# Kernel optimization log

Measured on AMD Instinct MI355X. Metric: run time of the kernel, lower is better.

The kernel has to match this reference:

```python
import jax, jax.numpy as jnp
import numpy as np

EPS = 1e-5  # BatchNorm2d default eps


def _conv3x3(x, w):
    # x: [B,C,H,W], w: [O,I,3,3], stride 1, 'same' padding (autopad k=3 -> p=1)
    return jax.lax.conv_general_dilated(
        x, w, window_strides=(1, 1), padding=((1, 1), (1, 1)),
        dimension_numbers=("NCHW", "OIHW", "NCHW"))


def _bn(x, g, b, m, v):
    # inference-mode BatchNorm2d with materialized running stats
    scale = (g / jnp.sqrt(v + EPS))[None, :, None, None]
    return (x - m[None, :, None, None]) * scale + b[None, :, None, None]


def _silu(x):
    return x * jax.nn.sigmoid(x)


def _pam(y, q_w, q_b, k_w, k_b, v_w, v_b, pam_gamma):
    # PAM_Module: full pixel-wise self-attention over N = H*W tokens
    B, C, H, W = y.shape
    N = H * W
    yf = y.reshape(B, C, N)
    # 1x1 convs expressed as channel matmuls; q_w: [C//8, C], v_w: [C, C]
    q = jnp.einsum("oc,bcn->bno", q_w, yf) + q_b                 # [B, N, C//8]
    k = jnp.einsum("oc,bcn->bon", k_w, yf) + k_b[None, :, None]  # [B, C//8, N]
    v = jnp.einsum("oc,bcn->bon", v_w, yf) + v_b[None, :, None]  # [B, C, N]
    energy = jnp.einsum("bno,bom->bnm", q, k)                    # [B, N, N]
    attn = jax.nn.softmax(energy, axis=-1)
    # torch: bmm(v, attn.permute(0,2,1)) -> out[b,c,n] = sum_m v[b,c,m] * attn[b,n,m]
    out = jnp.einsum("bcm,bnm->bcn", v, attn).reshape(B, C, H, W)
    return pam_gamma * out + y


def setup_inputs() -> dict:
    key = jax.random.key(0)
    ks = jax.random.split(key, 16)
    B, C1, C2, H, W = 4, 64, 64, 64, 64
    C_ = C2 // 2          # e = 0.5
    C8 = C2 // 8          # PAM q/k channels
    s = 0.05
    inp = {
        "x": jax.random.normal(ks[0], (B, C1, H, W), jnp.float32),
        # cv1: Conv(c1, c_, 3, 1)
        "cv1_w": jax.random.normal(ks[1], (C_, C1, 3, 3), jnp.float32) * s,
        "bn1_g": jax.random.uniform(ks[2], (C_,), jnp.float32, 0.5, 1.5),
        "bn1_b": jax.random.normal(ks[3], (C_,), jnp.float32) * s,
        "bn1_m": jax.random.normal(ks[4], (C_,), jnp.float32) * s,
        "bn1_v": jax.random.uniform(ks[5], (C_,), jnp.float32, 0.5, 1.5),
        # cv2: Conv(c_, c2, 3, 1)
        "cv2_w": jax.random.normal(ks[6], (C2, C_, 3, 3), jnp.float32) * s,
        "bn2_g": jax.random.uniform(ks[7], (C2,), jnp.float32, 0.5, 1.5),
        "bn2_b": jax.random.normal(ks[8], (C2,), jnp.float32) * s,
        "bn2_m": jax.random.normal(ks[9], (C2,), jnp.float32) * s,
        "bn2_v": jax.random.uniform(ks[10], (C2,), jnp.float32, 0.5, 1.5),
        # PAM 1x1 convs (flattened kernels) + biases + gamma
        "q_w": jax.random.normal(ks[11], (C8, C2), jnp.float32) * s,
        "q_b": jax.random.normal(ks[12], (C8,), jnp.float32) * s,
        "k_w": jax.random.normal(ks[13], (C8, C2), jnp.float32) * s,
        "k_b": jax.random.normal(ks[14], (C8,), jnp.float32) * s,
        "v_w": jax.random.normal(ks[15], (C2, C2), jnp.float32) * s,
        "v_b": jnp.zeros((C2,), jnp.float32),
        "pam_gamma": jnp.float32(0.5),  # torch inits 0 (identity); nonzero to exercise path
    }
    return inp


def reference(x, cv1_w, bn1_g, bn1_b, bn1_m, bn1_v,
              cv2_w, bn2_g, bn2_b, bn2_m, bn2_v,
              q_w, q_b, k_w, k_b, v_w, v_b, pam_gamma):
    y = _silu(_bn(_conv3x3(x, cv1_w), bn1_g, bn1_b, bn1_m, bn1_v))   # cv1
    y = _silu(_bn(_conv3x3(y, cv2_w), bn2_g, bn2_b, bn2_m, bn2_v))   # cv2
    # SAA: PAM applied twice on identical input and summed == 2 * PAM(y)
    att = 2.0 * _pam(y, q_w, q_b, k_w, k_b, v_w, v_b, pam_gamma)
    return x + att  # shortcut active (c1 == c2)
```

## Files before the change

### kernel.cpp

```cpp
#include <hip/hip_runtime.h>
#include <hip/hip_bf16.h>

#define NB 4
#define NN 4096

typedef short  bf16x8 __attribute__((ext_vector_type(8)));
typedef float  f32x4  __attribute__((ext_vector_type(4)));

static __device__ __forceinline__ ushort f2bf(float f) {
    unsigned u = __float_as_uint(f);
    u += 0x7fffu + ((u >> 16) & 1u);
    return (ushort)(u >> 16);
}
static __device__ __forceinline__ float bflo(unsigned w) { return __uint_as_float(w << 16); }
static __device__ __forceinline__ float bfhi(unsigned w) { return __uint_as_float(w & 0xffff0000u); }

__global__ __launch_bounds__(256) void prep(
    const float* __restrict__ x, const float* __restrict__ w1, const float* __restrict__ w2,
    ushort* __restrict__ xt, ushort* __restrict__ W1r, ushort* __restrict__ W2r)
{
    const int tid = threadIdx.x;
    const int blk = blockIdx.x;
    if (blk < 256) {
        __shared__ float Ts[64][66];
        const int b = blk >> 6, n0 = (blk & 63) * 64;
        const int wv = tid >> 6, lane = tid & 63;
        #pragma unroll
        for (int i = 0; i < 16; ++i) {
            int ci = i * 4 + wv, nn = lane;
            Ts[ci][nn] = x[((size_t)b * 64 + ci) * NN + n0 + nn];
        }
        __syncthreads();
        #pragma unroll
        for (int i = 0; i < 16; ++i) {
            int nn = i * 4 + wv, ci = lane;
            xt[((size_t)b * NN + n0 + nn) * 64 + ci] = f2bf(Ts[ci][nn]);
        }
    } else if (blk < 258) {
        const int base = (blk - 256) * 9216;
        #pragma unroll
        for (int i = 0; i < 36; ++i) {
            int e = base + i * 256 + tid;
            int co = e / 576, k = e % 576, tap = k >> 6, ci = k & 63;
            W1r[e] = f2bf(w1[((size_t)co * 64 + ci) * 9 + tap]);
        }
    } else {
        const int base = (blk - 258) * 9216;
        #pragma unroll
        for (int i = 0; i < 36; ++i) {
            int e = base + i * 256 + tid;
            int co = e / 288, k = e % 288, tap = k >> 5, ci = k & 31;
            W2r[e] = f2bf(w2[((size_t)co * 32 + ci) * 9 + tap]);
        }
    }
}

__global__ __launch_bounds__(256) void conv1_mfma(
    const ushort* __restrict__ xt, const ushort* __restrict__ W1r,
    const float* __restrict__ bng, const float* __restrict__ bnb,
    const float* __restrict__ bnm, const float* __restrict__ bnv,
    ushort* __restrict__ y1t)
{
    __shared__ __align__(16) ushort As[32 * 600];
    __shared__ __align__(16) ushort Xs[24 * 66 * 8];

    const int tid = threadIdx.x;
    const int h = blockIdx.x, b = blockIdx.y;

    #pragma unroll
    for (int i = 0; i < 9; ++i) {
        int cid = i * 256 + tid;
        int row = cid / 72, off = cid % 72;
        *(uint4*)&As[row * 600 + off * 8] = *(const uint4*)(W1r + (size_t)cid * 8);
    }
    #pragma unroll
    for (int r = 0; r < 3; ++r) {
        int gh = h - 1 + r;
        #pragma unroll
        for (int i = 0; i < 2; ++i) {
            int cid = i * 256 + tid;
            int w_ = cid >> 3, cc = cid & 7;
            uint4 v = {0, 0, 0, 0};
            if ((unsigned)gh < 64u)
                v = *(const uint4*)(xt + ((size_t)(b * NN + gh * 64) * 64) + (size_t)cid * 8);
            *(uint4*)&Xs[((r * 8 + cc) * 66 + (w_ + 1)) * 8] = v;
        }
    }
    if (tid < 48) {
        int r = tid >> 4, q = tid & 15, cc = q >> 1, side = (q & 1) * 65;
        uint4 z = {0, 0, 0, 0};
        *(uint4*)&Xs[((r * 8 + cc) * 66 + side) * 8] = z;
    }
    __syncthreads();

    const int lane = tid & 63, wv = tid >> 6;
    const int quad = lane >> 4, l15 = lane & 15;
    const int ch = wv & 1, ph = wv >> 1;

    f32x4 acc[2] = {{0.f,0.f,0.f,0.f},{0.f,0.f,0.f,0.f}};
    #pragma unroll
    for (int kk = 0; kk < 18; ++kk) {
        const int tap = kk >> 1;
        const int dyr = tap / 3, dx = tap % 3;
        bf16x8 af = *(const bf16x8*)&As[(ch * 16 + l15) * 600 + kk * 32 + quad * 8];
        #pragma unroll
        for (int s = 0; s < 2; ++s) {
            int p = ph * 32 + s * 16 + l15;
            bf16x8 bf = *(const bf16x8*)&Xs[((dyr * 8 + (kk & 1) * 4 + quad) * 66 + p + dx) * 8];
            acc[s] = __builtin_amdgcn_mfma_f32_16x16x32_bf16(af, bf, acc[s], 0, 0, 0);
        }
    }

    const int cb = ch * 16 + quad * 4;
    float sc[4], bs[4];
    #pragma unroll
    for (int r = 0; r < 4; ++r) {
        int co = cb + r;
        sc[r] = bng[co] / sqrtf(bnv[co] + 1e-5f);
        bs[r] = bnb[co] - bnm[co] * sc[r];
    }
    #pragma unroll
    for (int s = 0; s < 2; ++s) {
        int p = ph * 32 + s * 16 + l15;
        ushort u4[4];
        #pragma unroll
        for (int r = 0; r < 4; ++r) {
            float pre = acc[s][r] * sc[r] + bs[r];
            u4[r] = f2bf(pre / (1.f + __expf(-pre)));
        }
        *(uint2*)&y1t[((size_t)(b * NN + h * 64 + p)) * 32 + cb] = *(uint2*)u4;
    }
}

__global__ __launch_bounds__(256) void conv2qkv(
    const ushort* __restrict__ y1t, const ushort* __restrict__ W2r,
    const float* __restrict__ bng, const float* __restrict__ bnb,
    const float* __restrict__ bnm, const float* __restrict__ bnv,
    const float* __restrict__ qw, const float* __restrict__ qb,
    const float* __restrict__ kw, const float* __restrict__ kb,
    const float* __restrict__ vw, const float* __restrict__ vb,
    float* __restrict__ y, ushort* __restrict__ q8,
    ushort* __restrict__ ko, ushort* __restrict__ vt)
{
    __shared__ __align__(16) ushort As[64 * 312];
    __shared__ __align__(16) ushort Xs[12 * 66 * 8];
    __shared__ __align__(16) ushort Yt[64 * 76];
    __shared__ __align__(16) ushort Wq[80 * 76];
    __shared__ float Bv[80];

    const int tid = threadIdx.x;
    const int h = blockIdx.x, b = blockIdx.y;

    #pragma unroll
    for (int i = 0; i < 9; ++i) {
        int cid = i * 256 + tid;
        int row = cid / 36, off = cid % 36;
        *(uint4*)&As[row * 312 + off * 8] = *(const uint4*)(W2r + (size_t)cid * 8);
    }
    #pragma unroll
    for (int r = 0; r < 3; ++r) {
        int gh = h - 1 + r;
        int cid = tid;
        int w_ = cid >> 2, cc = cid & 3;
        uint4 v = {0, 0, 0, 0};
        if ((unsigned)gh < 64u)
            v = *(const uint4*)(y1t + ((size_t)(b * NN + gh * 64) * 32) + (size_t)cid * 8);
        *(uint4*)&Xs[((r * 4 + cc) * 66 + (w_ + 1)) * 8] = v;
    }
    if (tid < 24) {
        int r = tid >> 3, q = tid & 7, cc = q >> 1, side = (q & 1) * 65;
        uint4 z = {0, 0, 0, 0};
        *(uint4*)&Xs[((r * 4 + cc) * 66 + side) * 8] = z;
    }
    for (int i = tid; i < 2560; i += 256) {
        int chw = i >> 5, c2 = (i & 31) * 2;
        const float* src = (chw < 8) ? (qw + chw * 64 + c2)
                         : (chw < 16) ? (kw + (chw - 8) * 64 + c2)
                         : (vw + (chw - 16) * 64 + c2);
        float2 v2 = *(const float2*)src;
        *(unsigned*)&Wq[chw * 76 + c2] = ((unsigned)f2bf(v2.y) << 16) | f2bf(v2.x);
    }
    if (tid < 80) Bv[tid] = (tid < 8) ? qb[tid] : (tid < 16) ? kb[tid - 8] : vb[tid - 16];
    __syncthreads();

    const int lane = tid & 63, wv = tid >> 6;
    const int quad = lane >> 4, l15 = lane & 15;

    f32x4 acc[4] = {{0.f,0.f,0.f,0.f},{0.f,0.f,0.f,0.f},{0.f,0.f,0.f,0.f},{0.f,0.f,0.f,0.f}};
    #pragma unroll
    for (int kk = 0; kk < 9; ++kk) {
        const int dyr = kk / 3, dx = kk % 3;
        bf16x8 af = *(const bf16x8*)&As[(wv * 16 + l15) * 312 + kk * 32 + quad * 8];
        #pragma unroll
        for (int s = 0; s < 4; ++s) {
            int p = s * 16 + l15;
            bf16x8 bf = *(const bf16x8*)&Xs[((dyr * 4 + quad) * 66 + p + dx) * 8];
            acc[s] = __builtin_amdgcn_mfma_f32_16x16x32_bf16(af, bf, acc[s], 0, 0, 0);
        }
    }

    const int cb = wv * 16 + quad * 4;
    float sc[4], bs[4];
    #pragma unroll
    for (int r = 0; r < 4; ++r) {
        int co = cb + r;
        sc[r] = bng[co] / sqrtf(bnv[co] + 1e-5f);
        bs[r] = bnb[co] - bnm[co] * sc[r];
    }
    #pragma unroll
    for (int s = 0; s < 4; ++s) {
        int p = s * 16 + l15;
        #pragma unroll
        for (int r = 0; r < 4; ++r) {
            float pre = acc[s][r] * sc[r] + bs[r];
            float res = pre / (1.f + __expf(-pre));
            y[((size_t)(b * 64 + cb + r)) * NN + h * 64 + p] = res;
            Yt[p * 76 + cb + r] = f2bf(res);
        }
    }
    __syncthreads();

    bf16x8 aY0 = *(const bf16x8*)&Yt[(wv * 16 + l15) * 76 + quad * 8];
    bf16x8 aY1 = *(const bf16x8*)&Yt[(wv * 16 + l15) * 76 + 32 + quad * 8];
    const int nbase = h * 64 + wv * 16 + quad * 4;
    const int vslot = h * 64 + (wv >> 1) * 32 + quad * 8 + (wv & 1) * 4;
    #pragma unroll
    for (int cht = 0; cht < 5; ++cht) {
        bf16x8 bW0 = *(const bf16x8*)&Wq[(cht * 16 + l15) * 76 + quad * 8];
        bf16x8 bW1 = *(const bf16x8*)&Wq[(cht * 16 + l15) * 76 + 32 + quad * 8];
        f32x4 qa = {0.f, 0.f, 0.f, 0.f};
        qa = __builtin_amdgcn_mfma_f32_16x16x32_bf16(aY0, bW0, qa, 0, 0, 0);
        qa = __builtin_amdgcn_mfma_f32_16x16x32_bf16(aY1, bW1, qa, 0, 0, 0);
        const float bias = Bv[cht * 16 + l15];
        const int chn = cht * 16 + l15;
        if (cht == 0) {
            if (l15 < 8) {
                #pragma unroll
                for (int r = 0; r < 4; ++r)
                    q8[((size_t)b * NN + nbase + r) * 8 + chn] = f2bf(qa[r] + bias);
            } else {
                #pragma unroll
                for (int r = 0; r < 4; ++r)
                    ko[((size_t)b * NN + nbase + r) * 8 + (chn - 8)] = f2bf(qa[r] + bias);
            }
        } else {
            const int c = chn - 16;
            ushort u4[4];
            #pragma unroll
            for (int r = 0; r < 4; ++r) u4[r] = f2bf(qa[r] + bias);
            *(uint2*)&vt[((size_t)b * 64 + c) * NN + vslot] = *(uint2*)u4;
        }
    }
}

__global__ __launch_bounds__(256, 4) void flash_pam_split(
    const ushort* __restrict__ q8,
    const ushort* __restrict__ k8,
    const ushort* __restrict__ vt,
    ushort* __restrict__ O0, ushort* __restrict__ O1,
    float* __restrict__ lpart)
{
    __shared__ __align__(16) float Osum[4 * 2304];
    __shared__ float Lw[4][32];

    const int tid = threadIdx.x;
    const int bx = blockIdx.x;
    const int b  = bx >> 8;
    const int nt = (bx >> 1) & 127;
    const int sp = bx & 1;
    const int n0 = nt * 32;
    const int mb = sp * 2048;

    const int lane = tid & 63, w = tid >> 6;
    const int quad = lane >> 4, l15 = lane & 15;

    const uint4 z4 = {0u, 0u, 0u, 0u};

    bf16x8 bQ[2];
    #pragma unroll
    for (int af = 0; af < 2; ++af) {
        uint4 qv = *(const uint4*)(q8 + ((size_t)b * NN + n0 + af * 16 + l15) * 8);
        uint4 sel = (quad == 0) ? qv : z4;
        bQ[af] = *(bf16x8*)&sel;
    }

    const ushort* kg = k8 + ((size_t)b * NN + mb + w * 512) * 8;
    const ushort* vg = vt + (size_t)b * 64 * NN + mb + w * 512;

    f32x4 acc[2][4] = {{{0.f,0.f,0.f,0.f},{0.f,0.f,0.f,0.f},{0.f,0.f,0.f,0.f},{0.f,0.f,0.f,0.f}},
                       {{0.f,0.f,0.f,0.f},{0.f,0.f,0.f,0.f},{0.f,0.f,0.f,0.f},{0.f,0.f,0.f,0.f}}};
    float lacc[2] = {0.f, 0.f};
    const f32x4 zf = {0.f, 0.f, 0.f, 0.f};

    #pragma unroll 2
    for (int t = 0; t < 16; ++t) {
        const int g = t * 32;
        uint4 k0r = *(const uint4*)(kg + (size_t)(g + l15) * 8);
        uint4 k1r = *(const uint4*)(kg + (size_t)(g + 16 + l15) * 8);
        uint4 k0s = (quad == 0) ? k0r : z4;
        uint4 k1s = (quad == 0) ? k1r : z4;
        bf16x8 aK0 = *(bf16x8*)&k0s;
        bf16x8 aK1 = *(bf16x8*)&k1s;

        bf16x8 vb_[4];
        #pragma unroll
        for (int ct = 0; ct < 4; ++ct)
            vb_[ct] = *(const bf16x8*)(vg + (size_t)(ct * 16 + l15) * NN + g + quad * 8);

        f32x4 s0[2], s1[2];
        #pragma unroll
        for (int af = 0; af < 2; ++af) {
            s0[af] = __builtin_amdgcn_mfma_f32_16x16x32_bf16(aK0, bQ[af], zf, 0, 0, 0);
            s1[af] = __builtin_amdgcn_mfma_f32_16x16x32_bf16(aK1, bQ[af], zf, 0, 0, 0);
        }

        bf16x8 pa[2];
        #pragma unroll
        for (int af = 0; af < 2; ++af) {
            union { ushort u[8]; bf16x8 v; } pk;
            #pragma unroll
            for (int r = 0; r < 4; ++r) {
                float e = __expf(s0[af][r]);
                lacc[af] += e;
                pk.u[r] = f2bf(e);
            }
            #pragma unroll
            for (int r = 0; r < 4; ++r) {
                float e = __expf(s1[af][r]);
                lacc[af] += e;
                pk.u[4 + r] = f2bf(e);
            }
            pa[af] = pk.v;
        }

        #pragma unroll
        for (int af = 0; af < 2; ++af)
            #pragma unroll
            for (int ct = 0; ct < 4; ++ct)
                acc[af][ct] = __builtin_amdgcn_mfma_f32_16x16x32_bf16(pa[af], vb_[ct], acc[af][ct], 0, 0, 0);
    }

    #pragma unroll
    for (int af = 0; af < 2; ++af) {
        lacc[af] += __shfl_xor(lacc[af], 16, 64);
        lacc[af] += __shfl_xor(lacc[af], 32, 64);
    }
    if (quad == 0) {
        Lw[w][l15]      = lacc[0];
        Lw[w][16 + l15] = lacc[1];
    }

    #pragma unroll
    for (int af = 0; af < 2; ++af)
        #pragma unroll
        for (int ct = 0; ct < 4; ++ct)
            *(f32x4*)&Osum[w * 2304 + (ct * 16 + l15) * 36 + af * 16 + quad * 4] = acc[af][ct];
    __syncthreads();

    if (tid < 32)
        lpart[((size_t)(sp * 4 + b)) * NN + n0 + tid] =
            Lw[0][tid] + Lw[1][tid] + Lw[2][tid] + Lw[3][tid];

    ushort* Od = sp ? O1 : O0;
    const int nn = tid & 31, cq = tid >> 5;
    #pragma unroll
    for (int u = 0; u < 8; ++u) {
        int c = cq * 8 + u;
        float v = Osum[0 * 2304 + c * 36 + nn] + Osum[1 * 2304 + c * 36 + nn]
                + Osum[2 * 2304 + c * 36 + nn] + Osum[3 * 2304 + c * 36 + nn];
        Od[((size_t)b * 64 + c) * NN + n0 + nn] = f2bf(v);
    }
}

__global__ __launch_bounds__(256) void merge_out(
    const ushort* __restrict__ O0, const ushort* __restrict__ O1,
    const float* __restrict__ lpart,
    const float* __restrict__ x, const float* __restrict__ y,
    const float* __restrict__ gamma_p, float* __restrict__ out)
{
    const size_t base4 = ((size_t)blockIdx.x * 256 + threadIdx.x) * 4;
    const int n = (int)(base4 & 4095);
    const int b = (int)(base4 >> 18);
    const float g2 = 2.f * gamma_p[0];

    uint2 r0 = *(const uint2*)(O0 + base4);
    uint2 r1 = *(const uint2*)(O1 + base4);
    const float* l0 = lpart + (size_t)b * NN + n;
    const float* l1 = lpart + (size_t)(4 + b) * NN + n;

    f32x4 o;
    o[0] = bflo(r0.x) + bflo(r1.x);
    o[1] = bfhi(r0.x) + bfhi(r1.x);
    o[2] = bflo(r0.y) + bflo(r1.y);
    o[3] = bfhi(r0.y) + bfhi(r1.y);

    f32x4 xv = *(const f32x4*)(x + base4);
    f32x4 yv = *(const f32x4*)(y + base4);
    f32x4 res;
    #pragma unroll
    for (int u = 0; u < 4; ++u)
        res[u] = xv[u] + 2.f * yv[u] + g2 * o[u] / (l0[u] + l1[u]);
    *(f32x4*)(out + base4) = res;
}

extern "C" void kernel_launch(void* const* d_in, const int* in_sizes, int n_in,
                              void* d_out, int out_size, void* d_ws, size_t ws_size,
                              hipStream_t stream) {
    const float* x    = (const float*)d_in[0];
    const float* w1   = (const float*)d_in[1];
    const float* g1   = (const float*)d_in[2];
    const float* b1   = (const float*)d_in[3];
    const float* m1   = (const float*)d_in[4];
    const float* v1   = (const float*)d_in[5];
    const float* w2   = (const float*)d_in[6];
    const float* g2   = (const float*)d_in[7];
    const float* b2   = (const float*)d_in[8];
    const float* m2   = (const float*)d_in[9];
    const float* v2   = (const float*)d_in[10];
    const float* qw   = (const float*)d_in[11];
    const float* qb   = (const float*)d_in[12];
    const float* kw   = (const float*)d_in[13];
    const float* kb   = (const float*)d_in[14];
    const float* vw   = (const float*)d_in[15];
    const float* vb   = (const float*)d_in[16];
    const float* gam  = (const float*)d_in[17];
    float* outp = (float*)d_out;

    float* ws = (float*)d_ws;
    ushort* xt  = (ushort*)ws;
    float*  y   = ws + 524288;
    ushort* q8  = (ushort*)(ws + 1572864);
    ushort* kk  = (ushort*)(ws + 1703936);
    ushort* vv  = (ushort*)(ws + 1769472);
    float*  lp  = ws + 2293760;
    float*  S   = ws + 2326528;
    ushort* y1t = (ushort*)S;
    ushort* W1r = (ushort*)(S + 262144);
    ushort* W2r = (ushort*)(S + 271360);
    ushort* O0  = (ushort*)S;
    ushort* O1  = xt;

    prep<<<260, 256, 0, stream>>>(x, w1, w2, xt, W1r, W2r);
    conv1_mfma<<<dim3(64, NB), 256, 0, stream>>>(xt, W1r, g1, b1, m1, v1, y1t);
    conv2qkv<<<dim3(64, NB), 256, 0, stream>>>(y1t, W2r, g2, b2, m2, v2,
                                               qw, qb, kw, kb, vw, vb,
                                               y, q8, kk, vv);
    flash_pam_split<<<1024, 256, 0, stream>>>(q8, kk, vv, O0, O1, lp);
    merge_out<<<1024, 256, 0, stream>>>(O0, O1, lp, x, y, gam, outp);
}
```

Before: 149.8 us.

## Fuse split-KV merge and residual epilogue into single 8-wave flash PAM kernel

Replaces the two-way key split plus separate merge kernel with one kernel of 512 threads, where 8 waves each cover 512 keys and reduce their partial outputs and row sums in shared memory. The epilogue applies the normalization, gamma scaling and residual adds directly, removing the bf16 partial-output round trip through global memory and one kernel launch. In exchange the grid halves to 512 blocks of 512 threads and shared memory per block doubles to about 74 KB, which lowers occupancy and may leave compute units underused.

Measured after the change: 143.4 us. 4.3% less time.

```diff
diff --git a/kernel.cpp b/kernel.cpp
--- a/kernel.cpp
+++ b/kernel.cpp
@@ -12,8 +12,6 @@
     u += 0x7fffu + ((u >> 16) & 1u);
     return (ushort)(u >> 16);
 }
-static __device__ __forceinline__ float bflo(unsigned w) { return __uint_as_float(w << 16); }
-static __device__ __forceinline__ float bfhi(unsigned w) { return __uint_as_float(w & 0xffff0000u); }
 
 __global__ __launch_bounds__(256) void prep(
     const float* __restrict__ x, const float* __restrict__ w1, const float* __restrict__ w2,
@@ -253,23 +251,24 @@
     }
 }
 
-__global__ __launch_bounds__(256, 4) void flash_pam_split(
+__global__ __launch_bounds__(512, 4) void flash_pam(
     const ushort* __restrict__ q8,
     const ushort* __restrict__ k8,
     const ushort* __restrict__ vt,
-    ushort* __restrict__ O0, ushort* __restrict__ O1,
-    float* __restrict__ lpart)
+    const float* __restrict__ y,
+    const float* __restrict__ x,
+    const float* __restrict__ gamma_p,
+    float* __restrict__ out)
 {
-    __shared__ __align__(16) float Osum[4 * 2304];
-    __shared__ float Lw[4][32];
+    __shared__ __align__(16) float Osum[8 * 2304];
+    __shared__ float Lw[8][32];
+    __shared__ float Ls[32];
 
     const int tid = threadIdx.x;
     const int bx = blockIdx.x;
-    const int b  = bx >> 8;
-    const int nt = (bx >> 1) & 127;
-    const int sp = bx & 1;
+    const int b  = bx >> 7;
+    const int nt = bx & 127;
     const int n0 = nt * 32;
-    const int mb = sp * 2048;
 
     const int lane = tid & 63, w = tid >> 6;
     const int quad = lane >> 4, l15 = lane & 15;
@@ -284,8 +283,8 @@
         bQ[af] = *(bf16x8*)&sel;
     }
 
-    const ushort* kg = k8 + ((size_t)b * NN + mb + w * 512) * 8;
-    const ushort* vg = vt + (size_t)b * 64 * NN + mb + w * 512;
+    const ushort* kg = k8 + ((size_t)b * NN + w * 512) * 8;
+    const ushort* vg = vt + (size_t)b * 64 * NN + w * 512;
 
     f32x4 acc[2][4] = {{{0.f,0.f,0.f,0.f},{0.f,0.f,0.f,0.f},{0.f,0.f,0.f,0.f},{0.f,0.f,0.f,0.f}},
                        {{0.f,0.f,0.f,0.f},{0.f,0.f,0.f,0.f},{0.f,0.f,0.f,0.f},{0.f,0.f,0.f,0.f}}};
@@ -357,50 +356,26 @@
             *(f32x4*)&Osum[w * 2304 + (ct * 16 + l15) * 36 + af * 16 + quad * 4] = acc[af][ct];
     __syncthreads();
 
-    if (tid < 32)
-        lpart[((size_t)(sp * 4 + b)) * NN + n0 + tid] =
-            Lw[0][tid] + Lw[1][tid] + Lw[2][tid] + Lw[3][tid];
-
-    ushort* Od = sp ? O1 : O0;
-    const int nn = tid & 31, cq = tid >> 5;
-    #pragma unroll
-    for (int u = 0; u < 8; ++u) {
-        int c = cq * 8 + u;
-        float v = Osum[0 * 2304 + c * 36 + nn] + Osum[1 * 2304 + c * 36 + nn]
-                + Osum[2 * 2304 + c * 36 + nn] + Osum[3 * 2304 + c * 36 + nn];
-        Od[((size_t)b * 64 + c) * NN + n0 + nn] = f2bf(v);
-    }
-}
-
-__global__ __launch_bounds__(256) void merge_out(
-    const ushort* __restrict__ O0, const ushort* __restrict__ O1,
-    const float* __restrict__ lpart,
-    const float* __restrict__ x, const float* __restrict__ y,
-    const float* __restrict__ gamma_p, float* __restrict__ out)
-{
-    const size_t base4 = ((size_t)blockIdx.x * 256 + threadIdx.x) * 4;
-    const int n = (int)(base4 & 4095);
-    const int b = (int)(base4 >> 18);
-    const float g2 = 2.f * gamma_p[0];
-
-    uint2 r0 = *(const uint2*)(O0 + base4);
-    uint2 r1 = *(const uint2*)(O1 + base4);
-    const float* l0 = lpart + (size_t)b * NN + n;
-    const float* l1 = lpart + (size_t)(4 + b) * NN + n;
-
-    f32x4 o;
-    o[0] = bflo(r0.x) + bflo(r1.x);
-    o[1] = bfhi(r0.x) + bfhi(r1.x);
-    o[2] = bflo(r0.y) + bflo(r1.y);
-    o[3] = bfhi(r0.y) + bfhi(r1.y);
-
-    f32x4 xv = *(const f32x4*)(x + base4);
-    f32x4 yv = *(const f32x4*)(y + base4);
-    f32x4 res;
-    #pragma unroll
-    for (int u = 0; u < 4; ++u)
-        res[u] = xv[u] + 2.f * yv[u] + g2 * o[u] / (l0[u] + l1[u]);
-    *(f32x4*)(out + base4) = res;
+    if (tid < 32) Ls[tid] = Lw[0][tid] + Lw[1][tid] + Lw[2][tid] + Lw[3][tid]
+                          + Lw[4][tid] + Lw[5][tid] + Lw[6][tid] + Lw[7][tid];
+    __syncthreads();
+
+    {
+        const int c = tid >> 3, nn = (tid & 7) * 4;
+        f32x4 o = {0.f, 0.f, 0.f, 0.f};
+        #pragma unroll
+        for (int wv = 0; wv < 8; ++wv)
+            o += *(const f32x4*)&Osum[wv * 2304 + c * 36 + nn];
+        const float g2 = 2.f * gamma_p[0];
+        const size_t idx = ((size_t)b * 64 + c) * NN + n0 + nn;
+        f32x4 xv = *(const f32x4*)(x + idx);
+        f32x4 yv = *(const f32x4*)(y + idx);
+        f32x4 res;
+        #pragma unroll
+        for (int u = 0; u < 4; ++u)
+            res[u] = xv[u] + 2.f * yv[u] + g2 * o[u] / Ls[nn + u];
+        *(f32x4*)(out + idx) = res;
+    }
 }
 
 extern "C" void kernel_launch(void* const* d_in, const int* in_sizes, int n_in,
@@ -432,19 +407,15 @@
     ushort* q8  = (ushort*)(ws + 1572864);
     ushort* kk  = (ushort*)(ws + 1703936);
     ushort* vv  = (ushort*)(ws + 1769472);
-    float*  lp  = ws + 2293760;
     float*  S   = ws + 2326528;
     ushort* y1t = (ushort*)S;
     ushort* W1r = (ushort*)(S + 262144);
     ushort* W2r = (ushort*)(S + 271360);
-    ushort* O0  = (ushort*)S;
-    ushort* O1  = xt;
 
     prep<<<260, 256, 0, stream>>>(x, w1, w2, xt, W1r, W2r);
     conv1_mfma<<<dim3(64, NB), 256, 0, stream>>>(xt, W1r, g1, b1, m1, v1, y1t);
     conv2qkv<<<dim3(64, NB), 256, 0, stream>>>(y1t, W2r, g2, b2, m2, v2,
                                                qw, qb, kw, kb, vw, vb,
                                                y, q8, kk, vv);
-    flash_pam_split<<<1024, 256, 0, stream>>>(q8, kk, vv, O0, O1, lp);
-    merge_out<<<1024, 256, 0, stream>>>(O0, O1, lp, x, y, gam, outp);
-}
+    flash_pam<<<512, 512, 0, stream>>>(q8, kk, vv, y, x, gam, outp);
+}
```
